# Performance work log

Measured on AMD Instinct MI355X. Metric: run time of the kernel, lower is better.

The kernel has to match this reference:

```python
import jax, jax.numpy as jnp
import numpy as np

N = 100000   # nodes
E = 600000   # edges
D = 128      # in_dim == hidden
L = 3        # n_layers
B = 64       # graphs in batch


def setup_inputs() -> dict:
    key = jax.random.key(0)
    ks = jax.random.split(key, 7)
    x = jax.random.normal(ks[0], (N, D), dtype=jnp.float32)
    edge_index = jax.random.randint(ks[1], (2, E), 0, N, dtype=jnp.int32)
    batch_vec = jnp.sort(jax.random.randint(ks[2], (N,), 0, B, dtype=jnp.int32))
    scale = 1.0 / np.sqrt(D)
    Ws_self = jax.random.normal(ks[3], (L, D, D), dtype=jnp.float32) * scale
    bs_self = jax.random.normal(ks[4], (L, D), dtype=jnp.float32) * 0.01
    Ws_neigh = jax.random.normal(ks[5], (L, D, D), dtype=jnp.float32) * scale
    bs_neigh = jax.random.normal(ks[6], (L, D), dtype=jnp.float32) * 0.01
    return {"x": x, "edge_index": edge_index, "batch_vec": batch_vec,
            "Ws_self": Ws_self, "bs_self": bs_self,
            "Ws_neigh": Ws_neigh, "bs_neigh": bs_neigh}


def reference(x, edge_index, batch_vec, Ws_self, bs_self, Ws_neigh, bs_neigh):
    src, dst = edge_index[0], edge_index[1]
    # in-degree per node (clamped to 1), constant across layers
    deg = jax.ops.segment_sum(jnp.ones((E,), x.dtype), dst, num_segments=N)
    deg = jnp.maximum(deg, 1.0)[:, None]                     # [N, 1]
    for l in range(L):
        # gather neighbor features and scatter-mean onto dst nodes
        agg = jax.ops.segment_sum(x[src], dst, num_segments=N) / deg  # [N, D]
        h = x @ Ws_self[l] + bs_self[l] + agg @ Ws_neigh[l] + bs_neigh[l]
        x = jax.nn.relu(h)                                   # dropout: eval-mode identity
    # graph-level scatter_mean pooling
    pooled = jax.ops.segment_sum(x, batch_vec, num_segments=B)          # [B, D]
    cnt = jax.ops.segment_sum(jnp.ones((N,), x.dtype), batch_vec, num_segments=B)
    return pooled / jnp.maximum(cnt, 1.0)[:, None]
```

## Files before the change

kernel.cpp:

```cpp
#include <hip/hip_runtime.h>

#define N_NODES 100000
#define N_EDGES 600000
#define DIM     128
#define NGRAPHS 64
#define NPAD    100096
#define BCAP    32

typedef short  short8 __attribute__((ext_vector_type(8)));
typedef float  f32x4  __attribute__((ext_vector_type(4)));

__device__ __forceinline__ void atomAddF(float* p, float v) { unsafeAtomicAdd(p, v); }

__device__ __forceinline__ unsigned short f2bf(float f) {
    unsigned int u = __builtin_bit_cast(unsigned int, f);
    u += 0x7fffu + ((u >> 16) & 1u);
    return (unsigned short)(u >> 16);
}
__device__ __forceinline__ float bflo2f(unsigned int packed) {
    return __builtin_bit_cast(float, packed << 16);
}
__device__ __forceinline__ float bfhi2f(unsigned int packed) {
    return __builtin_bit_cast(float, packed & 0xffff0000u);
}

__global__ void cast_kernel(const float* __restrict__ x, unsigned short* __restrict__ xb) {
    int t = blockIdx.x * blockDim.x + threadIdx.x;
    size_t i8 = (size_t)t * 8;
    if (i8 >= (size_t)NPAD * DIM) return;
    uint4 o = make_uint4(0, 0, 0, 0);
    if (i8 < (size_t)N_NODES * DIM) {
        float4 v0 = *reinterpret_cast<const float4*>(x + i8);
        float4 v1 = *reinterpret_cast<const float4*>(x + i8 + 4);
        o.x = (unsigned)f2bf(v0.x) | ((unsigned)f2bf(v0.y) << 16);
        o.y = (unsigned)f2bf(v0.z) | ((unsigned)f2bf(v0.w) << 16);
        o.z = (unsigned)f2bf(v1.x) | ((unsigned)f2bf(v1.y) << 16);
        o.w = (unsigned)f2bf(v1.z) | ((unsigned)f2bf(v1.w) << 16);
    }
    *reinterpret_cast<uint4*>(xb + i8) = o;
}

__global__ void prep_kernel(const float* __restrict__ Ws, const float* __restrict__ Wn,
                            const float* __restrict__ bs, const float* __restrict__ bn,
                            unsigned short* __restrict__ Btg, float* __restrict__ biasg) {
    int t = blockIdx.x * blockDim.x + threadIdx.x;
    if (t >= 3 * 128 * 256) return;
    int layer = t >> 15;
    int rem   = t & 32767;
    int k     = rem >> 7;
    int col   = rem & 127;
    float w = (k < 128) ? Ws[layer * 16384 + k * 128 + col]
                        : Wn[layer * 16384 + (k - 128) * 128 + col];
    Btg[layer * 32768 + col * 256 + (k ^ ((col & 7) << 3))] = f2bf(w);
    if (t < 3 * 128) {
        biasg[t] = bs[t] + bn[t];
    }
}

__global__ void fill_kernel(const int* __restrict__ src, const int* __restrict__ dst,
                            int* __restrict__ bucket, int* __restrict__ cursor) {
    int t = blockIdx.x * blockDim.x + threadIdx.x;
    if (t >= N_EDGES) return;
    int d = dst[t];
    int pos = atomicAdd(&cursor[d], 1);
    if (pos < BCAP) bucket[d * BCAP + pos] = src[t];
}

__global__ void cnt_kernel(const int* __restrict__ batch, int* __restrict__ cnt) {
    __shared__ int bins[NGRAPHS];
    if (threadIdx.x < NGRAPHS) bins[threadIdx.x] = 0;
    __syncthreads();
    int t = blockIdx.x * blockDim.x + threadIdx.x;
    if (t < N_NODES) atomicAdd(&bins[batch[t]], 1);
    __syncthreads();
    if (threadIdx.x < NGRAPHS && bins[threadIdx.x] != 0)
        atomicAdd(&cnt[threadIdx.x], bins[threadIdx.x]);
}

__launch_bounds__(256)
__global__ void gather_kernel(const unsigned short* __restrict__ x,
                              const int* __restrict__ bucket,
                              const int* __restrict__ cursor,
                              unsigned short* __restrict__ agg) {
    const int l16  = threadIdx.x & 15;
    const int node = blockIdx.x * 16 + (threadIdx.x >> 4);
    const int k = min(cursor[node], BCAP);
    const int* __restrict__ bl = bucket + (size_t)node * BCAP;
    float acc[8];
#pragma unroll
    for (int i = 0; i < 8; ++i) acc[i] = 0.f;
    for (int j = 0; j < k; ++j) {
        int s = bl[j];
        uint4 v = *reinterpret_cast<const uint4*>(x + (size_t)s * DIM + l16 * 8);
        acc[0] += bflo2f(v.x); acc[1] += bfhi2f(v.x);
        acc[2] += bflo2f(v.y); acc[3] += bfhi2f(v.y);
        acc[4] += bflo2f(v.z); acc[5] += bfhi2f(v.z);
        acc[6] += bflo2f(v.w); acc[7] += bfhi2f(v.w);
    }
    const float inv = (k > 0) ? 1.0f / (float)k : 0.0f;
    uint4 o;
    o.x = (unsigned)f2bf(acc[0] * inv) | ((unsigned)f2bf(acc[1] * inv) << 16);
    o.y = (unsigned)f2bf(acc[2] * inv) | ((unsigned)f2bf(acc[3] * inv) << 16);
    o.z = (unsigned)f2bf(acc[4] * inv) | ((unsigned)f2bf(acc[5] * inv) << 16);
    o.w = (unsigned)f2bf(acc[6] * inv) | ((unsigned)f2bf(acc[7] * inv) << 16);
    *reinterpret_cast<uint4*>(agg + (size_t)node * DIM + l16 * 8) = o;
}

__launch_bounds__(512, 4)
__global__ void gemm_kernel(const unsigned short* __restrict__ X,
                            unsigned short* AGG,
                            const unsigned short* __restrict__ Btg,
                            const float* __restrict__ biasg) {
    __shared__ unsigned short Blds[128 * 256];

    const int tid  = threadIdx.x;
#pragma unroll
    for (int i = 0; i < 8; ++i) {
        int idx8 = (i * 512 + tid) * 8;
        *reinterpret_cast<uint4*>(Blds + idx8) =
            *reinterpret_cast<const uint4*>(Btg + idx8);
    }
    __syncthreads();

    const int wave = tid >> 6;
    const int lane = tid & 63;
    const int l15  = lane & 15;
    const int lk   = lane >> 4;
    const int row_base = blockIdx.x * 256 + wave * 32;

    float bias[8];
#pragma unroll
    for (int c = 0; c < 8; ++c) bias[c] = biasg[c * 16 + l15];

    f32x4 acc[2][8];
#pragma unroll
    for (int r = 0; r < 2; ++r)
#pragma unroll
        for (int c = 0; c < 8; ++c) acc[r][c] = (f32x4)0.f;

#pragma unroll 2
    for (int s = 0; s < 8; ++s) {
        const unsigned short* __restrict__ base = (s < 4) ? X : AGG;
        const int kofs = (s & 3) * 32 + lk * 8;
        short8 a0 = *reinterpret_cast<const short8*>(base + (size_t)(row_base + l15) * DIM + kofs);
        short8 a1 = *reinterpret_cast<const short8*>(base + (size_t)(row_base + 16 + l15) * DIM + kofs);
        const int kidx = s * 32 + lk * 8;
#pragma unroll
        for (int c = 0; c < 8; ++c) {
            int col = c * 16 + l15;
            short8 b = *reinterpret_cast<const short8*>(Blds + col * 256 + (kidx ^ ((col & 7) << 3)));
            acc[0][c] = __builtin_amdgcn_mfma_f32_16x16x32_bf16(a0, b, acc[0][c], 0, 0, 0);
            acc[1][c] = __builtin_amdgcn_mfma_f32_16x16x32_bf16(a1, b, acc[1][c], 0, 0, 0);
        }
    }

#pragma unroll
    for (int r = 0; r < 2; ++r) {
#pragma unroll
        for (int j = 0; j < 4; ++j) {
            int row = row_base + r * 16 + lk * 4 + j;
#pragma unroll
            for (int c = 0; c < 8; ++c) {
                float v = fmaxf(acc[r][c][j] + bias[c], 0.f);
                AGG[(size_t)row * DIM + c * 16 + l15] = f2bf(v);
            }
        }
    }
}

__global__ void pool_kernel(const unsigned short* __restrict__ x,
                            const int* __restrict__ batch,
                            float* __restrict__ out) {
    int q = threadIdx.x;
    int node0 = blockIdx.x * 32;
    float local = 0.0f;
    int prev = batch[node0];
    for (int nd = node0; nd < node0 + 32; ++nd) {
        int b = batch[nd];
        if (b != prev) {
            atomAddF(&out[prev * DIM + q], local);
            local = 0.0f;
            prev = b;
        }
        local += bflo2f((unsigned int)x[(size_t)nd * DIM + q]);
    }
    atomAddF(&out[prev * DIM + q], local);
}

__global__ void div_kernel(float* __restrict__ out, const int* __restrict__ cnt) {
    int t = blockIdx.x * blockDim.x + threadIdx.x;
    if (t < NGRAPHS * DIM) out[t] *= 1.0f / (float)max(cnt[t >> 7], 1);
}

extern "C" void kernel_launch(void* const* d_in, const int* in_sizes, int n_in,
                              void* d_out, int out_size, void* d_ws, size_t ws_size,
                              hipStream_t stream) {
    const float* x        = (const float*)d_in[0];
    const int*   ei       = (const int*)d_in[1];
    const int*   src      = ei;
    const int*   dst      = ei + N_EDGES;
    const int*   batch    = (const int*)d_in[2];
    const float* Ws_self  = (const float*)d_in[3];
    const float* bs_self  = (const float*)d_in[4];
    const float* Ws_neigh = (const float*)d_in[5];
    const float* bs_neigh = (const float*)d_in[6];
    float* out = (float*)d_out;

    const size_t NB = (size_t)NPAD * DIM;
    unsigned short* xb     = (unsigned short*)d_ws;
    unsigned short* b0     = xb + NB;
    unsigned short* b1     = b0 + NB;
    unsigned short* Btg    = b1 + NB;
    float*          biasg  = (float*)(Btg + 3 * 32768);
    int*            bucket = (int*)(biasg + 384);
    int*            cursor = bucket + (size_t)NPAD * BCAP;
    int*            cnt    = cursor + NPAD;

    hipMemsetAsync(cursor, 0, (NPAD + NGRAPHS) * sizeof(int), stream);
    hipMemsetAsync(out, 0, (size_t)NGRAPHS * DIM * sizeof(float), stream);

    cast_kernel<<<(int)((NB / 8 + 255) / 256), 256, 0, stream>>>(x, xb);
    prep_kernel<<<384, 256, 0, stream>>>(Ws_self, Ws_neigh, bs_self, bs_neigh, Btg, biasg);
    fill_kernel<<<(N_EDGES + 255) / 256, 256, 0, stream>>>(src, dst, bucket, cursor);
    cnt_kernel<<<(N_NODES + 255) / 256, 256, 0, stream>>>(batch, cnt);

    const int ga_grid = NPAD / 16;
    const int gm_grid = NPAD / 256;

    gather_kernel<<<ga_grid, 256, 0, stream>>>(xb, bucket, cursor, b1);
    gemm_kernel<<<gm_grid, 512, 0, stream>>>(xb, b1, Btg, biasg);
    gather_kernel<<<ga_grid, 256, 0, stream>>>(b1, bucket, cursor, b0);
    gemm_kernel<<<gm_grid, 512, 0, stream>>>(b1, b0, Btg + 32768, biasg + 128);
    gather_kernel<<<ga_grid, 256, 0, stream>>>(b0, bucket, cursor, b1);
    gemm_kernel<<<gm_grid, 512, 0, stream>>>(b0, b1, Btg + 65536, biasg + 256);

    pool_kernel<<<N_NODES / 32, DIM, 0, stream>>>(b1, batch, out);
    div_kernel<<<(NGRAPHS * DIM + 255) / 256, 256, 0, stream>>>(out, cnt);
}
```

Measured before the change: 299.0 us.

## Fuse setup kernels, unroll gather loads, drop LDS weight staging in GEMM

Zeroing of the cursor, count and output buffers moves into the cast kernel, replacing the two memsets. The fill and count kernels merge into one launch. The gather loop is unrolled four-way with an int4 index load, so more neighbour-row loads are in flight at once. The GEMM drops LDS staging of the weights and reads them straight from global memory through the cache. It also swaps the MFMA operands so each lane writes four contiguous outputs as one packed store, and uses 256-thread blocks over 128 rows. This removes launch and LDS-fill overhead, but the weight reads now depend on cache hit rates.

```diff
diff --git a/kernel.cpp b/kernel.cpp
--- a/kernel.cpp
+++ b/kernel.cpp
@@ -24,8 +24,13 @@
     return __builtin_bit_cast(float, packed & 0xffff0000u);
 }
 
-__global__ void cast_kernel(const float* __restrict__ x, unsigned short* __restrict__ xb) {
-    int t = blockIdx.x * blockDim.x + threadIdx.x;
+__global__ void cast_kernel(const float* __restrict__ x, unsigned short* __restrict__ xb,
+                            int* __restrict__ cursor, int* __restrict__ cnt,
+                            float* __restrict__ outz) {
+    int t = blockIdx.x * blockDim.x + threadIdx.x;
+    if (t < NPAD) cursor[t] = 0;
+    if (t < NGRAPHS) cnt[t] = 0;
+    if (t < NGRAPHS * DIM) outz[t] = 0.0f;
     size_t i8 = (size_t)t * 8;
     if (i8 >= (size_t)NPAD * DIM) return;
     uint4 o = make_uint4(0, 0, 0, 0);
@@ -51,26 +56,22 @@
     int col   = rem & 127;
     float w = (k < 128) ? Ws[layer * 16384 + k * 128 + col]
                         : Wn[layer * 16384 + (k - 128) * 128 + col];
-    Btg[layer * 32768 + col * 256 + (k ^ ((col & 7) << 3))] = f2bf(w);
-    if (t < 3 * 128) {
-        biasg[t] = bs[t] + bn[t];
-    }
-}
-
-__global__ void fill_kernel(const int* __restrict__ src, const int* __restrict__ dst,
-                            int* __restrict__ bucket, int* __restrict__ cursor) {
-    int t = blockIdx.x * blockDim.x + threadIdx.x;
-    if (t >= N_EDGES) return;
-    int d = dst[t];
-    int pos = atomicAdd(&cursor[d], 1);
-    if (pos < BCAP) bucket[d * BCAP + pos] = src[t];
-}
-
-__global__ void cnt_kernel(const int* __restrict__ batch, int* __restrict__ cnt) {
+    Btg[layer * 32768 + col * 256 + k] = f2bf(w);
+    if (t < 3 * 128) biasg[t] = bs[t] + bn[t];
+}
+
+__global__ void fillcnt_kernel(const int* __restrict__ src, const int* __restrict__ dst,
+                               int* __restrict__ bucket, int* __restrict__ cursor,
+                               const int* __restrict__ batch, int* __restrict__ cnt) {
     __shared__ int bins[NGRAPHS];
     if (threadIdx.x < NGRAPHS) bins[threadIdx.x] = 0;
     __syncthreads();
     int t = blockIdx.x * blockDim.x + threadIdx.x;
+    if (t < N_EDGES) {
+        int d = dst[t];
+        int pos = atomicAdd(&cursor[d], 1);
+        if (pos < BCAP) bucket[d * BCAP + pos] = src[t];
+    }
     if (t < N_NODES) atomicAdd(&bins[batch[t]], 1);
     __syncthreads();
     if (threadIdx.x < NGRAPHS && bins[threadIdx.x] != 0)
@@ -86,12 +87,30 @@
     const int node = blockIdx.x * 16 + (threadIdx.x >> 4);
     const int k = min(cursor[node], BCAP);
     const int* __restrict__ bl = bucket + (size_t)node * BCAP;
+    const size_t co = (size_t)l16 * 8;
     float acc[8];
 #pragma unroll
     for (int i = 0; i < 8; ++i) acc[i] = 0.f;
-    for (int j = 0; j < k; ++j) {
+
+    int j = 0;
+    for (; j + 4 <= k; j += 4) {
+        int4 s4 = *reinterpret_cast<const int4*>(bl + j);
+        uint4 v0 = *reinterpret_cast<const uint4*>(x + (size_t)s4.x * DIM + co);
+        uint4 v1 = *reinterpret_cast<const uint4*>(x + (size_t)s4.y * DIM + co);
+        uint4 v2 = *reinterpret_cast<const uint4*>(x + (size_t)s4.z * DIM + co);
+        uint4 v3 = *reinterpret_cast<const uint4*>(x + (size_t)s4.w * DIM + co);
+        acc[0] += bflo2f(v0.x) + bflo2f(v1.x) + bflo2f(v2.x) + bflo2f(v3.x);
+        acc[1] += bfhi2f(v0.x) + bfhi2f(v1.x) + bfhi2f(v2.x) + bfhi2f(v3.x);
+        acc[2] += bflo2f(v0.y) + bflo2f(v1.y) + bflo2f(v2.y) + bflo2f(v3.y);
+        acc[3] += bfhi2f(v0.y) + bfhi2f(v1.y) + bfhi2f(v2.y) + bfhi2f(v3.y);
+        acc[4] += bflo2f(v0.z) + bflo2f(v1.z) + bflo2f(v2.z) + bflo2f(v3.z);
+        acc[5] += bfhi2f(v0.z) + bfhi2f(v1.z) + bfhi2f(v2.z) + bfhi2f(v3.z);
+        acc[6] += bflo2f(v0.w) + bflo2f(v1.w) + bflo2f(v2.w) + bflo2f(v3.w);
+        acc[7] += bfhi2f(v0.w) + bfhi2f(v1.w) + bfhi2f(v2.w) + bfhi2f(v3.w);
+    }
+    for (; j < k; ++j) {
         int s = bl[j];
-        uint4 v = *reinterpret_cast<const uint4*>(x + (size_t)s * DIM + l16 * 8);
+        uint4 v = *reinterpret_cast<const uint4*>(x + (size_t)s * DIM + co);
         acc[0] += bflo2f(v.x); acc[1] += bfhi2f(v.x);
         acc[2] += bflo2f(v.y); acc[3] += bfhi2f(v.y);
         acc[4] += bflo2f(v.z); acc[5] += bfhi2f(v.z);
@@ -103,34 +122,25 @@
     o.y = (unsigned)f2bf(acc[2] * inv) | ((unsigned)f2bf(acc[3] * inv) << 16);
     o.z = (unsigned)f2bf(acc[4] * inv) | ((unsigned)f2bf(acc[5] * inv) << 16);
     o.w = (unsigned)f2bf(acc[6] * inv) | ((unsigned)f2bf(acc[7] * inv) << 16);
-    *reinterpret_cast<uint4*>(agg + (size_t)node * DIM + l16 * 8) = o;
-}
-
-__launch_bounds__(512, 4)
+    *reinterpret_cast<uint4*>(agg + (size_t)node * DIM + co) = o;
+}
+
+__launch_bounds__(256)
 __global__ void gemm_kernel(const unsigned short* __restrict__ X,
                             unsigned short* AGG,
                             const unsigned short* __restrict__ Btg,
                             const float* __restrict__ biasg) {
-    __shared__ unsigned short Blds[128 * 256];
-
     const int tid  = threadIdx.x;
-#pragma unroll
-    for (int i = 0; i < 8; ++i) {
-        int idx8 = (i * 512 + tid) * 8;
-        *reinterpret_cast<uint4*>(Blds + idx8) =
-            *reinterpret_cast<const uint4*>(Btg + idx8);
-    }
-    __syncthreads();
-
     const int wave = tid >> 6;
     const int lane = tid & 63;
     const int l15  = lane & 15;
     const int lk   = lane >> 4;
-    const int row_base = blockIdx.x * 256 + wave * 32;
-
-    float bias[8];
-#pragma unroll
-    for (int c = 0; c < 8; ++c) bias[c] = biasg[c * 16 + l15];
+    const int row_base = blockIdx.x * 128 + wave * 32;
+
+    f32x4 bias4[8];
+#pragma unroll
+    for (int c = 0; c < 8; ++c)
+        bias4[c] = *reinterpret_cast<const f32x4*>(biasg + c * 16 + lk * 4);
 
     f32x4 acc[2][8];
 #pragma unroll
@@ -147,23 +157,25 @@
         const int kidx = s * 32 + lk * 8;
 #pragma unroll
         for (int c = 0; c < 8; ++c) {
-            int col = c * 16 + l15;
-            short8 b = *reinterpret_cast<const short8*>(Blds + col * 256 + (kidx ^ ((col & 7) << 3)));
-            acc[0][c] = __builtin_amdgcn_mfma_f32_16x16x32_bf16(a0, b, acc[0][c], 0, 0, 0);
-            acc[1][c] = __builtin_amdgcn_mfma_f32_16x16x32_bf16(a1, b, acc[1][c], 0, 0, 0);
+            short8 b = *reinterpret_cast<const short8*>(Btg + (c * 16 + l15) * 256 + kidx);
+            acc[0][c] = __builtin_amdgcn_mfma_f32_16x16x32_bf16(b, a0, acc[0][c], 0, 0, 0);
+            acc[1][c] = __builtin_amdgcn_mfma_f32_16x16x32_bf16(b, a1, acc[1][c], 0, 0, 0);
         }
     }
 
 #pragma unroll
     for (int r = 0; r < 2; ++r) {
-#pragma unroll
-        for (int j = 0; j < 4; ++j) {
-            int row = row_base + r * 16 + lk * 4 + j;
-#pragma unroll
-            for (int c = 0; c < 8; ++c) {
-                float v = fmaxf(acc[r][c][j] + bias[c], 0.f);
-                AGG[(size_t)row * DIM + c * 16 + l15] = f2bf(v);
-            }
+        const size_t rowoff = (size_t)(row_base + r * 16 + l15) * DIM;
+#pragma unroll
+        for (int c = 0; c < 8; ++c) {
+            float f0 = fmaxf(acc[r][c][0] + bias4[c][0], 0.f);
+            float f1 = fmaxf(acc[r][c][1] + bias4[c][1], 0.f);
+            float f2 = fmaxf(acc[r][c][2] + bias4[c][2], 0.f);
+            float f3 = fmaxf(acc[r][c][3] + bias4[c][3], 0.f);
+            uint2 o;
+            o.x = (unsigned)f2bf(f0) | ((unsigned)f2bf(f1) << 16);
+            o.y = (unsigned)f2bf(f2) | ((unsigned)f2bf(f3) << 16);
+            *reinterpret_cast<uint2*>(AGG + rowoff + c * 16 + lk * 4) = o;
         }
     }
 }
@@ -216,23 +228,19 @@
     int*            cursor = bucket + (size_t)NPAD * BCAP;
     int*            cnt    = cursor + NPAD;
 
-    hipMemsetAsync(cursor, 0, (NPAD + NGRAPHS) * sizeof(int), stream);
-    hipMemsetAsync(out, 0, (size_t)NGRAPHS * DIM * sizeof(float), stream);
-
-    cast_kernel<<<(int)((NB / 8 + 255) / 256), 256, 0, stream>>>(x, xb);
+    cast_kernel<<<(int)((NB / 8 + 255) / 256), 256, 0, stream>>>(x, xb, cursor, cnt, out);
     prep_kernel<<<384, 256, 0, stream>>>(Ws_self, Ws_neigh, bs_self, bs_neigh, Btg, biasg);
-    fill_kernel<<<(N_EDGES + 255) / 256, 256, 0, stream>>>(src, dst, bucket, cursor);
-    cnt_kernel<<<(N_NODES + 255) / 256, 256, 0, stream>>>(batch, cnt);
+    fillcnt_kernel<<<(N_EDGES + 255) / 256, 256, 0, stream>>>(src, dst, bucket, cursor, batch, cnt);
 
     const int ga_grid = NPAD / 16;
-    const int gm_grid = NPAD / 256;
+    const int gm_grid = NPAD / 128;
 
     gather_kernel<<<ga_grid, 256, 0, stream>>>(xb, bucket, cursor, b1);
-    gemm_kernel<<<gm_grid, 512, 0, stream>>>(xb, b1, Btg, biasg);
+    gemm_kernel<<<gm_grid, 256, 0, stream>>>(xb, b1, Btg, biasg);
     gather_kernel<<<ga_grid, 256, 0, stream>>>(b1, bucket, cursor, b0);
-    gemm_kernel<<<gm_grid, 512, 0, stream>>>(b1, b0, Btg + 32768, biasg + 128);
+    gemm_kernel<<<gm_grid, 256, 0, stream>>>(b1, b0, Btg + 32768, biasg + 128);
     gather_kernel<<<ga_grid, 256, 0, stream>>>(b0, bucket, cursor, b1);
-    gemm_kernel<<<gm_grid, 512, 0, stream>>>(b0, b1, Btg + 65536, biasg + 256);
+    gemm_kernel<<<gm_grid, 256, 0, stream>>>(b0, b1, Btg + 65536, biasg + 256);
 
     pool_kernel<<<N_NODES / 32, DIM, 0, stream>>>(b1, batch, out);
     div_kernel<<<(NGRAPHS * DIM + 255) / 256, 256, 0, stream>>>(out, cnt);
```

Measured after the change: 363.6 us. +21.6%, slower.
